# Kernel optimization log

Measured on AMD Instinct MI355X. Metric: run time of the kernel, lower is better.

## Reference

```python
import jax, jax.numpy as jnp
import numpy as np

N = 1_000_000
NUM_CLASSES = 80
ALPHA = 0.25
GAMMA = 2.0
CENTER_W = 0.1
EPS = 1e-7  # torchvision generalized_box_iou_loss eps


def _make_boxes(u):
    # u: [N,4] uniform in [0,1) -> valid xyxy boxes inside ~1024x1024 canvas
    x1 = u[:, 0] * 1024.0
    y1 = u[:, 1] * 1024.0
    x2 = x1 + u[:, 2] * 256.0 + 1.0
    y2 = y1 + u[:, 3] * 256.0 + 1.0
    return jnp.stack([x1, y1, x2, y2], axis=-1)


def setup_inputs() -> dict:
    key = jax.random.key(0)
    k1, k2, k3, k4, k5 = jax.random.split(key, 5)
    cls_logits = jax.random.normal(k1, (N, NUM_CLASSES), dtype=jnp.float32)
    bbox_reg = _make_boxes(jax.random.uniform(k2, (N, 4), dtype=jnp.float32))
    centerness = jax.random.normal(k3, (N,), dtype=jnp.float32)
    gt_bboxes = _make_boxes(jax.random.uniform(k4, (N, 4), dtype=jnp.float32))
    gt_classes = jax.random.randint(k5, (N,), 0, NUM_CLASSES, dtype=jnp.int32)
    return {"cls_logits": cls_logits, "bbox_reg": bbox_reg,
            "centerness": centerness, "gt_bboxes": gt_bboxes,
            "gt_classes": gt_classes}


def _giou_loss_mean(pred, gt):
    # elementwise pairwise GIoU loss, mean reduction (torchvision semantics)
    px1, py1, px2, py2 = pred[:, 0], pred[:, 1], pred[:, 2], pred[:, 3]
    gx1, gy1, gx2, gy2 = gt[:, 0], gt[:, 1], gt[:, 2], gt[:, 3]
    iw = jnp.clip(jnp.minimum(px2, gx2) - jnp.maximum(px1, gx1), 0.0)
    ih = jnp.clip(jnp.minimum(py2, gy2) - jnp.maximum(py1, gy1), 0.0)
    inter = iw * ih
    area_p = (px2 - px1) * (py2 - py1)
    area_g = (gx2 - gx1) * (gy2 - gy1)
    union = area_p + area_g - inter
    iou = inter / (union + EPS)
    cw = jnp.maximum(px2, gx2) - jnp.minimum(px1, gx1)
    ch = jnp.maximum(py2, gy2) - jnp.minimum(py1, gy1)
    area_c = cw * ch
    giou = iou - (area_c - union) / (area_c + EPS)
    return jnp.mean(1.0 - giou)


def reference(cls_logits, bbox_reg, centerness, gt_bboxes, gt_classes):
    # focal loss built from standard cross-entropy (as in the torch module)
    logp = jax.nn.log_softmax(cls_logits, axis=-1)            # [N, C]
    ce = -jnp.take_along_axis(logp, gt_classes[:, None].astype(jnp.int32), axis=1)[:, 0]
    pt = jnp.exp(-ce)
    focal_loss = jnp.mean(ALPHA * (1.0 - pt) ** GAMMA * ce)

    iou_loss = _giou_loss_mean(bbox_reg, gt_bboxes)

    # BCE-with-logits vs all-ones target: mean(softplus(-x))
    center_loss = jnp.mean(jnp.logaddexp(0.0, -centerness))

    total = focal_loss + iou_loss + CENTER_W * center_loss
    return total, focal_loss, iou_loss, center_loss
```

## Files before the change

kernel.cpp:

```cpp
#include <hip/hip_runtime.h>
#include <math.h>

#define NUM_CLASSES 80
#define FLOAT4_PER_ROW (NUM_CLASSES / 4)

constexpr float ALPHA = 0.25f;
constexpr float CENTER_W = 0.1f;
constexpr float EPS_GIOU = 1e-7f;

__global__ __launch_bounds__(256) void hdm_loss_kernel(
    const float* __restrict__ cls_logits,
    const float* __restrict__ bbox_reg,
    const float* __restrict__ centerness,
    const float* __restrict__ gt_bboxes,
    const int*   __restrict__ gt_classes,
    double* __restrict__ partials,
    int n)
{
    const int row = blockIdx.x * blockDim.x + threadIdx.x;

    float focal_t = 0.0f, giou_t = 0.0f, center_t = 0.0f;

    if (row < n) {
        const float4* lp = (const float4*)(cls_logits + (size_t)row * NUM_CLASSES);
        float4 v[FLOAT4_PER_ROW];
        #pragma unroll
        for (int j = 0; j < FLOAT4_PER_ROW; ++j) v[j] = lp[j];

        float m = -INFINITY;
        #pragma unroll
        for (int j = 0; j < FLOAT4_PER_ROW; ++j) {
            m = fmaxf(m, fmaxf(fmaxf(v[j].x, v[j].y), fmaxf(v[j].z, v[j].w)));
        }
        float s = 0.0f;
        #pragma unroll
        for (int j = 0; j < FLOAT4_PER_ROW; ++j) {
            s += __expf(v[j].x - m);
            s += __expf(v[j].y - m);
            s += __expf(v[j].z - m);
            s += __expf(v[j].w - m);
        }
        const int gc = gt_classes[row];
        const float xg = cls_logits[(size_t)row * NUM_CLASSES + gc];
        const float lse = m + __logf(s);
        const float ce  = lse - xg;
        const float pt  = __expf(-ce);
        const float omp = 1.0f - pt;
        focal_t = ALPHA * omp * omp * ce;

        const float4 p = ((const float4*)bbox_reg)[row];
        const float4 g = ((const float4*)gt_bboxes)[row];
        const float iw = fmaxf(fminf(p.z, g.z) - fmaxf(p.x, g.x), 0.0f);
        const float ih = fmaxf(fminf(p.w, g.w) - fmaxf(p.y, g.y), 0.0f);
        const float inter  = iw * ih;
        const float area_p = (p.z - p.x) * (p.w - p.y);
        const float area_g = (g.z - g.x) * (g.w - g.y);
        const float uni    = area_p + area_g - inter;
        const float iou    = inter / (uni + EPS_GIOU);
        const float cw = fmaxf(p.z, g.z) - fminf(p.x, g.x);
        const float ch = fmaxf(p.w, g.w) - fminf(p.y, g.y);
        const float area_c = cw * ch;
        const float giou = iou - (area_c - uni) / (area_c + EPS_GIOU);
        giou_t = 1.0f - giou;

        const float c = centerness[row];
        center_t = fmaxf(-c, 0.0f) + log1pf(__expf(-fabsf(c)));
    }

    double f = (double)focal_t, gi = (double)giou_t, ce_ = (double)center_t;
    #pragma unroll
    for (int off = 32; off > 0; off >>= 1) {
        f   += __shfl_down(f,   off, 64);
        gi  += __shfl_down(gi,  off, 64);
        ce_ += __shfl_down(ce_, off, 64);
    }
    __shared__ double sf[4], sg[4], sc[4];
    const int lane = threadIdx.x & 63;
    const int wave = threadIdx.x >> 6;
    if (lane == 0) { sf[wave] = f; sg[wave] = gi; sc[wave] = ce_; }
    __syncthreads();
    if (threadIdx.x == 0) {
        double tf = 0.0, tg = 0.0, tc = 0.0;
        #pragma unroll
        for (int w = 0; w < 4; ++w) { tf += sf[w]; tg += sg[w]; tc += sc[w]; }
        partials[blockIdx.x * 3 + 0] = tf;
        partials[blockIdx.x * 3 + 1] = tg;
        partials[blockIdx.x * 3 + 2] = tc;
    }
}

__global__ __launch_bounds__(256) void hdm_finalize_kernel(
    const double* __restrict__ partials, int nblocks, int n,
    float* __restrict__ out)
{
    double f = 0.0, g = 0.0, c = 0.0;
    for (int i = threadIdx.x; i < nblocks; i += 256) {
        f += partials[i * 3 + 0];
        g += partials[i * 3 + 1];
        c += partials[i * 3 + 2];
    }
    #pragma unroll
    for (int off = 32; off > 0; off >>= 1) {
        f += __shfl_down(f, off, 64);
        g += __shfl_down(g, off, 64);
        c += __shfl_down(c, off, 64);
    }
    __shared__ double sf[4], sg[4], sc[4];
    const int lane = threadIdx.x & 63;
    const int wave = threadIdx.x >> 6;
    if (lane == 0) { sf[wave] = f; sg[wave] = g; sc[wave] = c; }
    __syncthreads();
    if (threadIdx.x == 0) {
        double tf = 0.0, tg = 0.0, tc = 0.0;
        #pragma unroll
        for (int w = 0; w < 4; ++w) { tf += sf[w]; tg += sg[w]; tc += sc[w]; }
        const double inv_n = 1.0 / (double)n;
        const double focal_mean  = tf * inv_n;
        const double iou_mean    = tg * inv_n;
        const double center_mean = tc * inv_n;
        const double total = focal_mean + iou_mean + (double)CENTER_W * center_mean;
        out[0] = (float)total;
        out[1] = (float)focal_mean;
        out[2] = (float)iou_mean;
        out[3] = (float)center_mean;
    }
}

extern "C" void kernel_launch(void* const* d_in, const int* in_sizes, int n_in,
                              void* d_out, int out_size, void* d_ws, size_t ws_size,
                              hipStream_t stream) {
    const float* cls_logits = (const float*)d_in[0];
    const float* bbox_reg   = (const float*)d_in[1];
    const float* centerness = (const float*)d_in[2];
    const float* gt_bboxes  = (const float*)d_in[3];
    const int*   gt_classes = (const int*)d_in[4];
    float* out = (float*)d_out;

    const int n = in_sizes[2];
    const int nblocks = (n + 255) / 256;
    double* partials = (double*)d_ws;

    hdm_loss_kernel<<<nblocks, 256, 0, stream>>>(
        cls_logits, bbox_reg, centerness, gt_bboxes, gt_classes, partials, n);
    hdm_finalize_kernel<<<1, 256, 0, stream>>>(partials, nblocks, n, out);
}
```

Baseline: 454.5 us.

## Stage logits through LDS with coalesced float4 loads per block

Each block now loads its 128 rows of logits cooperatively, with consecutive threads reading consecutive float4s, and writes them into a padded shared-memory tile. Each thread then computes its row's softmax and target logit from that tile, which removes the strided per-thread row loads and the extra global gather for the target class. Block size drops to 128 threads. The cost is about 43KB of LDS per block, which limits occupancy, plus one extra barrier.

```diff
diff --git a/kernel.cpp b/kernel.cpp
--- a/kernel.cpp
+++ b/kernel.cpp
@@ -2,13 +2,16 @@
 #include <math.h>
 
 #define NUM_CLASSES 80
-#define FLOAT4_PER_ROW (NUM_CLASSES / 4)
+#define F4_PER_ROW  20
+#define ROWS_PER_BLOCK 128
+#define THREADS 128
+#define ROW_STRIDE 84
 
 constexpr float ALPHA = 0.25f;
 constexpr float CENTER_W = 0.1f;
 constexpr float EPS_GIOU = 1e-7f;
 
-__global__ __launch_bounds__(256) void hdm_loss_kernel(
+__global__ __launch_bounds__(THREADS) void hdm_loss_kernel(
     const float* __restrict__ cls_logits,
     const float* __restrict__ bbox_reg,
     const float* __restrict__ centerness,
@@ -17,31 +20,49 @@
     double* __restrict__ partials,
     int n)
 {
-    const int row = blockIdx.x * blockDim.x + threadIdx.x;
+    __shared__ float tile[ROWS_PER_BLOCK * ROW_STRIDE];
+
+    const int t = threadIdx.x;
+    const int row_base = blockIdx.x * ROWS_PER_BLOCK;
+    const int row = row_base + t;
+
+    const int total_f4 = n * F4_PER_ROW;
+    const int slab_base = row_base * F4_PER_ROW;
+    const float4* src = (const float4*)cls_logits;
+    #pragma unroll
+    for (int k = 0; k < F4_PER_ROW; ++k) {
+        const int F = k * THREADS + t;
+        const int gF = slab_base + F;
+        if (gF < total_f4) {
+            const float4 v = src[gF];
+            const int lrow = F / F4_PER_ROW;
+            const int c4   = F % F4_PER_ROW;
+            *(float4*)&tile[lrow * ROW_STRIDE + c4 * 4] = v;
+        }
+    }
+    __syncthreads();
 
     float focal_t = 0.0f, giou_t = 0.0f, center_t = 0.0f;
 
     if (row < n) {
-        const float4* lp = (const float4*)(cls_logits + (size_t)row * NUM_CLASSES);
-        float4 v[FLOAT4_PER_ROW];
-        #pragma unroll
-        for (int j = 0; j < FLOAT4_PER_ROW; ++j) v[j] = lp[j];
-
+        const float4* myrow = (const float4*)&tile[t * ROW_STRIDE];
         float m = -INFINITY;
         #pragma unroll
-        for (int j = 0; j < FLOAT4_PER_ROW; ++j) {
-            m = fmaxf(m, fmaxf(fmaxf(v[j].x, v[j].y), fmaxf(v[j].z, v[j].w)));
+        for (int j = 0; j < F4_PER_ROW; ++j) {
+            const float4 v = myrow[j];
+            m = fmaxf(m, fmaxf(fmaxf(v.x, v.y), fmaxf(v.z, v.w)));
         }
         float s = 0.0f;
         #pragma unroll
-        for (int j = 0; j < FLOAT4_PER_ROW; ++j) {
-            s += __expf(v[j].x - m);
-            s += __expf(v[j].y - m);
-            s += __expf(v[j].z - m);
-            s += __expf(v[j].w - m);
+        for (int j = 0; j < F4_PER_ROW; ++j) {
+            const float4 v = myrow[j];
+            s += __expf(v.x - m);
+            s += __expf(v.y - m);
+            s += __expf(v.z - m);
+            s += __expf(v.w - m);
         }
         const int gc = gt_classes[row];
-        const float xg = cls_logits[(size_t)row * NUM_CLASSES + gc];
+        const float xg = tile[t * ROW_STRIDE + gc];
         const float lse = m + __logf(s);
         const float ce  = lse - xg;
         const float pt  = __expf(-ce);
@@ -74,18 +95,15 @@
         gi  += __shfl_down(gi,  off, 64);
         ce_ += __shfl_down(ce_, off, 64);
     }
-    __shared__ double sf[4], sg[4], sc[4];
-    const int lane = threadIdx.x & 63;
-    const int wave = threadIdx.x >> 6;
+    __shared__ double sf[2], sg[2], sc[2];
+    const int lane = t & 63;
+    const int wave = t >> 6;
     if (lane == 0) { sf[wave] = f; sg[wave] = gi; sc[wave] = ce_; }
     __syncthreads();
-    if (threadIdx.x == 0) {
-        double tf = 0.0, tg = 0.0, tc = 0.0;
-        #pragma unroll
-        for (int w = 0; w < 4; ++w) { tf += sf[w]; tg += sg[w]; tc += sc[w]; }
-        partials[blockIdx.x * 3 + 0] = tf;
-        partials[blockIdx.x * 3 + 1] = tg;
-        partials[blockIdx.x * 3 + 2] = tc;
+    if (t == 0) {
+        partials[blockIdx.x * 3 + 0] = sf[0] + sf[1];
+        partials[blockIdx.x * 3 + 1] = sg[0] + sg[1];
+        partials[blockIdx.x * 3 + 2] = sc[0] + sc[1];
     }
 }
 
@@ -137,10 +155,10 @@
     float* out = (float*)d_out;
 
     const int n = in_sizes[2];
-    const int nblocks = (n + 255) / 256;
+    const int nblocks = (n + ROWS_PER_BLOCK - 1) / ROWS_PER_BLOCK;
     double* partials = (double*)d_ws;
 
-    hdm_loss_kernel<<<nblocks, 256, 0, stream>>>(
+    hdm_loss_kernel<<<nblocks, THREADS, 0, stream>>>(
         cls_logits, bbox_reg, centerness, gt_bboxes, gt_classes, partials, n);
     hdm_finalize_kernel<<<1, 256, 0, stream>>>(partials, nblocks, n, out);
 }
```

Measured after the change: 515.5 us. 13.4% more time.

## Split each logits row across four lanes for coalesced loads, grid-stride loops

Applied to the files above, without the earlier changes.

Four threads now cooperate on each 80-class row, each loading interleaved float4 chunks so that wave loads are contiguous. Row max and sum are reduced with xor shuffles, and the target logit is selected in registers and fetched from its owning lane with a shuffle instead of a second global load. The kernel uses a fixed 4096-block grid-stride layout with nontemporal loads, and the box and centerness terms run in a separate per-element loop. This adds shuffle overhead and a fixed grid size, in exchange for much better memory coalescing.

```diff
diff --git a/kernel.cpp b/kernel.cpp
--- a/kernel.cpp
+++ b/kernel.cpp
@@ -2,13 +2,18 @@
 #include <math.h>
 
 #define NUM_CLASSES 80
-#define FLOAT4_PER_ROW (NUM_CLASSES / 4)
+#define F4_PER_ROW  20
+#define THREADS     256
+#define NBLOCKS     4096
+#define ROWS_PER_BLOCK_A (THREADS / 4)
 
 constexpr float ALPHA = 0.25f;
 constexpr float CENTER_W = 0.1f;
 constexpr float EPS_GIOU = 1e-7f;
 
-__global__ __launch_bounds__(256) void hdm_loss_kernel(
+typedef float f32x4 __attribute__((ext_vector_type(4)));
+
+__global__ __launch_bounds__(THREADS) void hdm_loss_kernel(
     const float* __restrict__ cls_logits,
     const float* __restrict__ bbox_reg,
     const float* __restrict__ centerness,
@@ -17,75 +22,109 @@
     double* __restrict__ partials,
     int n)
 {
-    const int row = blockIdx.x * blockDim.x + threadIdx.x;
+    const int t = threadIdx.x;
+    double f_acc = 0.0, g_acc = 0.0, c_acc = 0.0;
 
-    float focal_t = 0.0f, giou_t = 0.0f, center_t = 0.0f;
+    {
+        const int q = t >> 2;
+        const int c = t & 3;
+        const f32x4* src = (const f32x4*)cls_logits;
 
-    if (row < n) {
-        const float4* lp = (const float4*)(cls_logits + (size_t)row * NUM_CLASSES);
-        float4 v[FLOAT4_PER_ROW];
-        #pragma unroll
-        for (int j = 0; j < FLOAT4_PER_ROW; ++j) v[j] = lp[j];
+        for (int rb = blockIdx.x * ROWS_PER_BLOCK_A; rb < n;
+             rb += NBLOCKS * ROWS_PER_BLOCK_A) {
+            const int row = rb + q;
+            const bool live = (row < n);
 
-        float m = -INFINITY;
-        #pragma unroll
-        for (int j = 0; j < FLOAT4_PER_ROW; ++j) {
-            m = fmaxf(m, fmaxf(fmaxf(v[j].x, v[j].y), fmaxf(v[j].z, v[j].w)));
+            f32x4 v[5];
+            const long base = (long)row * F4_PER_ROW + c;
+            #pragma unroll
+            for (int j = 0; j < 5; ++j) {
+                v[j] = live ? __builtin_nontemporal_load(&src[base + j * 4])
+                            : (f32x4){0.f, 0.f, 0.f, 0.f};
+            }
+            const int gc = live ? gt_classes[row] : 0;
+
+            float m = -INFINITY;
+            #pragma unroll
+            for (int j = 0; j < 5; ++j)
+                m = fmaxf(m, fmaxf(fmaxf(v[j].x, v[j].y), fmaxf(v[j].z, v[j].w)));
+            m = fmaxf(m, __shfl_xor(m, 1, 64));
+            m = fmaxf(m, __shfl_xor(m, 2, 64));
+
+            float s = 0.0f;
+            #pragma unroll
+            for (int j = 0; j < 5; ++j) {
+                s += __expf(v[j].x - m);
+                s += __expf(v[j].y - m);
+                s += __expf(v[j].z - m);
+                s += __expf(v[j].w - m);
+            }
+            s += __shfl_xor(s, 1, 64);
+            s += __shfl_xor(s, 2, 64);
+
+            const int j_src = gc >> 4;
+            const int comp  = gc & 3;
+            float sel = 0.0f;
+            #pragma unroll
+            for (int j = 0; j < 5; ++j) {
+                const f32x4 vv = v[j];
+                const float cand = (comp == 0) ? vv.x :
+                                   (comp == 1) ? vv.y :
+                                   (comp == 2) ? vv.z : vv.w;
+                sel = (j == j_src) ? cand : sel;
+            }
+            const int lane = t & 63;
+            const float xg = __shfl(sel, (lane & ~3) | ((gc >> 2) & 3), 64);
+
+            if (live && c == 0) {
+                const float lse = m + __logf(s);
+                const float ce  = lse - xg;
+                const float pt  = __expf(-ce);
+                const float omp = 1.0f - pt;
+                f_acc += (double)(ALPHA * omp * omp * ce);
+            }
         }
-        float s = 0.0f;
-        #pragma unroll
-        for (int j = 0; j < FLOAT4_PER_ROW; ++j) {
-            s += __expf(v[j].x - m);
-            s += __expf(v[j].y - m);
-            s += __expf(v[j].z - m);
-            s += __expf(v[j].w - m);
-        }
-        const int gc = gt_classes[row];
-        const float xg = cls_logits[(size_t)row * NUM_CLASSES + gc];
-        const float lse = m + __logf(s);
-        const float ce  = lse - xg;
-        const float pt  = __expf(-ce);
-        const float omp = 1.0f - pt;
-        focal_t = ALPHA * omp * omp * ce;
-
-        const float4 p = ((const float4*)bbox_reg)[row];
-        const float4 g = ((const float4*)gt_bboxes)[row];
-        const float iw = fmaxf(fminf(p.z, g.z) - fmaxf(p.x, g.x), 0.0f);
-        const float ih = fmaxf(fminf(p.w, g.w) - fmaxf(p.y, g.y), 0.0f);
-        const float inter  = iw * ih;
-        const float area_p = (p.z - p.x) * (p.w - p.y);
-        const float area_g = (g.z - g.x) * (g.w - g.y);
-        const float uni    = area_p + area_g - inter;
-        const float iou    = inter / (uni + EPS_GIOU);
-        const float cw = fmaxf(p.z, g.z) - fminf(p.x, g.x);
-        const float ch = fmaxf(p.w, g.w) - fminf(p.y, g.y);
-        const float area_c = cw * ch;
-        const float giou = iou - (area_c - uni) / (area_c + EPS_GIOU);
-        giou_t = 1.0f - giou;
-
-        const float c = centerness[row];
-        center_t = fmaxf(-c, 0.0f) + log1pf(__expf(-fabsf(c)));
     }
 
-    double f = (double)focal_t, gi = (double)giou_t, ce_ = (double)center_t;
+    {
+        const f32x4* pb = (const f32x4*)bbox_reg;
+        const f32x4* gb = (const f32x4*)gt_bboxes;
+        for (int i = blockIdx.x * THREADS + t; i < n; i += NBLOCKS * THREADS) {
+            const f32x4 p = __builtin_nontemporal_load(&pb[i]);
+            const f32x4 g = __builtin_nontemporal_load(&gb[i]);
+            const float iw = fmaxf(fminf(p.z, g.z) - fmaxf(p.x, g.x), 0.0f);
+            const float ih = fmaxf(fminf(p.w, g.w) - fmaxf(p.y, g.y), 0.0f);
+            const float inter  = iw * ih;
+            const float area_p = (p.z - p.x) * (p.w - p.y);
+            const float area_g = (g.z - g.x) * (g.w - g.y);
+            const float uni    = area_p + area_g - inter;
+            const float iou    = inter / (uni + EPS_GIOU);
+            const float cw = fmaxf(p.z, g.z) - fminf(p.x, g.x);
+            const float ch = fmaxf(p.w, g.w) - fminf(p.y, g.y);
+            const float area_c = cw * ch;
+            const float giou = iou - (area_c - uni) / (area_c + EPS_GIOU);
+            g_acc += (double)(1.0f - giou);
+
+            const float cc = centerness[i];
+            c_acc += (double)(fmaxf(-cc, 0.0f) + log1pf(__expf(-fabsf(cc))));
+        }
+    }
+
     #pragma unroll
     for (int off = 32; off > 0; off >>= 1) {
-        f   += __shfl_down(f,   off, 64);
-        gi  += __shfl_down(gi,  off, 64);
-        ce_ += __shfl_down(ce_, off, 64);
+        f_acc += __shfl_down(f_acc, off, 64);
+        g_acc += __shfl_down(g_acc, off, 64);
+        c_acc += __shfl_down(c_acc, off, 64);
     }
     __shared__ double sf[4], sg[4], sc[4];
-    const int lane = threadIdx.x & 63;
-    const int wave = threadIdx.x >> 6;
-    if (lane == 0) { sf[wave] = f; sg[wave] = gi; sc[wave] = ce_; }
+    const int lane = t & 63;
+    const int wave = t >> 6;
+    if (lane == 0) { sf[wave] = f_acc; sg[wave] = g_acc; sc[wave] = c_acc; }
     __syncthreads();
-    if (threadIdx.x == 0) {
-        double tf = 0.0, tg = 0.0, tc = 0.0;
-        #pragma unroll
-        for (int w = 0; w < 4; ++w) { tf += sf[w]; tg += sg[w]; tc += sc[w]; }
-        partials[blockIdx.x * 3 + 0] = tf;
-        partials[blockIdx.x * 3 + 1] = tg;
-        partials[blockIdx.x * 3 + 2] = tc;
+    if (t == 0) {
+        partials[blockIdx.x * 3 + 0] = sf[0] + sf[1] + sf[2] + sf[3];
+        partials[blockIdx.x * 3 + 1] = sg[0] + sg[1] + sg[2] + sg[3];
+        partials[blockIdx.x * 3 + 2] = sc[0] + sc[1] + sc[2] + sc[3];
     }
 }
 
@@ -137,10 +176,9 @@
     float* out = (float*)d_out;
 
     const int n = in_sizes[2];
-    const int nblocks = (n + 255) / 256;
     double* partials = (double*)d_ws;
 
-    hdm_loss_kernel<<<nblocks, 256, 0, stream>>>(
+    hdm_loss_kernel<<<NBLOCKS, THREADS, 0, stream>>>(
         cls_logits, bbox_reg, centerness, gt_bboxes, gt_classes, partials, n);
-    hdm_finalize_kernel<<<1, 256, 0, stream>>>(partials, nblocks, n, out);
+    hdm_finalize_kernel<<<1, 256, 0, stream>>>(partials, NBLOCKS, n, out);
 }
```

Result: faster. 443.4 us (-2.4%).
